# Kernel tuning notes

Measured on AMD Instinct MI355X. Metric: run time of the kernel, lower is better.

## Reference

```python
import jax, jax.numpy as jnp
import numpy as np

N = 50000
E = 800000
HEADS = 4
C = 64  # per-head channels
IN = 256
NEG_SLOPE = 0.2


def setup_inputs() -> dict:
    key = jax.random.key(0)
    k = jax.random.split(key, 6)
    x = jax.random.normal(k[0], (N, IN), dtype=jnp.float32)
    edge_index = jax.random.randint(k[1], (2, E), 0, N, dtype=jnp.int64)
    # Glorot-ish scale for weights
    W = jax.random.normal(k[2], (IN, HEADS * C), dtype=jnp.float32) * (1.0 / np.sqrt(IN))
    att_src = jax.random.normal(k[3], (HEADS, C), dtype=jnp.float32) * (1.0 / np.sqrt(C))
    att_dst = jax.random.normal(k[4], (HEADS, C), dtype=jnp.float32) * (1.0 / np.sqrt(C))
    bias = jax.random.normal(k[5], (HEADS * C,), dtype=jnp.float32) * 0.02
    return {"x": x, "edge_index": edge_index, "W": W, "att_src": att_src,
            "att_dst": att_dst, "bias": bias}


def _gat_forward(x, edge_index, W, att_src, att_dst, bias):
    n = x.shape[0]
    h = (x @ W).reshape(n, HEADS, C)  # [N, H, C]

    # add self loops (PyG default add_self_loops=True)
    loop = jnp.arange(n, dtype=edge_index.dtype)
    src = jnp.concatenate([edge_index[0], loop])  # [E+N]
    dst = jnp.concatenate([edge_index[1], loop])

    # per-node attention contributions  [N, H]
    a_src = jnp.einsum('nhc,hc->nh', h, att_src)
    a_dst = jnp.einsum('nhc,hc->nh', h, att_dst)

    # edge logits with leaky relu  [E+N, H]
    logits = a_src[src] + a_dst[dst]
    logits = jnp.where(logits >= 0, logits, NEG_SLOPE * logits)

    # segment softmax over destination neighborhoods
    seg_max = jax.ops.segment_max(logits, dst, num_segments=n)  # [N, H]
    seg_max = jnp.where(jnp.isfinite(seg_max), seg_max, 0.0)
    ex = jnp.exp(logits - seg_max[dst])
    denom = jax.ops.segment_sum(ex, dst, num_segments=n)  # [N, H]
    alpha = ex / (denom[dst] + 1e-16)  # [E+N, H]

    # weighted scatter-add of source messages
    msgs = alpha[:, :, None] * h[src]  # [E+N, H, C]
    out = jax.ops.segment_sum(msgs, dst, num_segments=n)  # [N, H, C]
    out = out.reshape(n, HEADS * C) + bias
    return jax.nn.relu(out)


def reference(x, edge_index, W, att_src, att_dst, bias):
    return _gat_forward(x, edge_index, W, att_src, att_dst, bias)
```

## Files before the change

kernel.cpp:

```cpp
#include <hip/hip_runtime.h>
#include <hip/hip_bf16.h>
#include <math.h>

#define NEG 0.2f
#define BSH 6
#define EPB 4096

typedef __attribute__((ext_vector_type(4))) float f4;
typedef __attribute__((ext_vector_type(8))) short s8;

__device__ __forceinline__ short f2bf(float f) {
    unsigned u = __float_as_uint(f);
    u += 0x7fff + ((u >> 16) & 1);
    return (short)(u >> 16);
}
__device__ __forceinline__ unsigned pk2(float a, float b) {
    union { __hip_bfloat162 h; unsigned u; } c;
    c.h = __float22bfloat162_rn(make_float2(a, b));
    return c.u;
}
__device__ __forceinline__ float bf2f(unsigned short s) {
    return __uint_as_float(((unsigned)s) << 16);
}

__global__ __launch_bounds__(256) void prep_count(
    const float* __restrict__ W, short* __restrict__ Wt, int* __restrict__ off,
    const int* __restrict__ ei, int* __restrict__ hist2d,
    int E, int N, int NBUCK, int NB, int Etot)
{
    const int blk = blockIdx.x, t = threadIdx.x;
    if (blk < 256) {
        int id = blk * 256 + t;
        int n = id >> 8, k = id & 255;
        Wt[id] = f2bf(W[k * 256 + n]);
        if (id == 0) off[N] = Etot;
        return;
    }
    extern __shared__ int lh[];
    const int cblk = blk - 256;
    for (int b = t; b < NBUCK; b += 256) lh[b] = 0;
    __syncthreads();
    const int e0 = cblk * EPB;
    if (e0 + EPB <= E) {
#pragma unroll
        for (int i = 0; i < EPB / 1024; ++i) {
            int e = e0 + i * 1024 + t * 4;
            int4 d = *(const int4*)(ei + E + e);
            atomicAdd(&lh[d.x >> BSH], 1);
            atomicAdd(&lh[d.y >> BSH], 1);
            atomicAdd(&lh[d.z >> BSH], 1);
            atomicAdd(&lh[d.w >> BSH], 1);
        }
    } else {
        for (int i = 0; i < EPB / 256; ++i) {
            int e = e0 + i * 256 + t;
            if (e < Etot) {
                int dte = (e < E) ? ei[E + e] : (e - E);
                atomicAdd(&lh[dte >> BSH], 1);
            }
        }
    }
    __syncthreads();
    for (int b = t; b < NBUCK; b += 256) hist2d[b * NB + cblk] = lh[b];
}

__global__ __launch_bounds__(1024) void scan1(const int* __restrict__ src,
                                              int* __restrict__ dstT,
                                              int* __restrict__ bsum,
                                              int Ntot, int NB, int NBUCK)
{
    __shared__ int wsum[16], wexc[16];
    const int t = threadIdx.x, lane = t & 63, w = t >> 6;
    const int idx = blockIdx.x * 1024 + t;
    int v = (idx < Ntot) ? src[idx] : 0;
    int val = v;
#pragma unroll
    for (int o = 1; o < 64; o <<= 1) {
        int u = __shfl_up(val, o);
        if (lane >= o) val += u;
    }
    if (lane == 63) wsum[w] = val;
    __syncthreads();
    if (t < 16) {
        int s = wsum[t];
#pragma unroll
        for (int o = 1; o < 16; o <<= 1) {
            int u = __shfl_up(s, o, 16);
            if (t >= o) s += u;
        }
        wexc[t] = s - wsum[t];
        if (t == 15) bsum[blockIdx.x] = s;
    }
    __syncthreads();
    if (idx < Ntot) {
        int b = idx / NB, cblk = idx - b * NB;
        dstT[(size_t)cblk * NBUCK + b] = wexc[w] + val - v;
    }
}

__device__ __forceinline__ void bexc_scan_wave(const int* __restrict__ bsum,
                                               int* bexc_l, int NCH, int t)
{
    if (t < 64) {
        int carry = 0;
        for (int base = 0; base < NCH; base += 64) {
            int i = base + t;
            int v = (i < NCH) ? bsum[i] : 0;
            int val = v;
#pragma unroll
            for (int o = 1; o < 64; o <<= 1) {
                int u = __shfl_up(val, o);
                if (t >= o) val += u;
            }
            if (i < NCH) bexc_l[i] = carry + val - v;
            carry += __shfl(val, 63);
        }
    }
}

__global__ __launch_bounds__(512) void gemm_scatter(
    const float* __restrict__ x, const short* __restrict__ Wt,
    const float* __restrict__ att_src, const float* __restrict__ att_dst,
    short* __restrict__ hb, float* __restrict__ a_src_n,
    float* __restrict__ a_dst_n, int M,
    const int* __restrict__ ei, const int* __restrict__ scannedT,
    const int* __restrict__ bsum, unsigned* __restrict__ bucketed,
    int E, int N, int NBUCK, int NB, int NCH)
{
    extern __shared__ __align__(16) char smem[];
    const int t = threadIdx.x;

    if (blockIdx.x < NB) {
        int* bexc_l = (int*)smem;
        int* lcur   = (int*)smem + 256;
        const int cblk = blockIdx.x;
        bexc_scan_wave(bsum, bexc_l, NCH, t);
        __syncthreads();
        const int* srow = scannedT + (size_t)cblk * NBUCK;
        for (int b = t; b < NBUCK; b += 512)
            lcur[b] = srow[b] + bexc_l[(b * NB + cblk) >> 10];
        __syncthreads();
        const int e0 = cblk * EPB, Etot = E + N;
        if (e0 + EPB <= E) {
#pragma unroll
            for (int i = 0; i < EPB / 2048; ++i) {
                int e = e0 + i * 2048 + t * 4;
                int4 s4 = *(const int4*)(ei + e);
                int4 d4 = *(const int4*)(ei + E + e);
                int p0 = atomicAdd(&lcur[d4.x >> BSH], 1);
                bucketed[p0] = (unsigned)s4.x | ((unsigned)(d4.x & 63) << 20);
                int p1 = atomicAdd(&lcur[d4.y >> BSH], 1);
                bucketed[p1] = (unsigned)s4.y | ((unsigned)(d4.y & 63) << 20);
                int p2 = atomicAdd(&lcur[d4.z >> BSH], 1);
                bucketed[p2] = (unsigned)s4.z | ((unsigned)(d4.z & 63) << 20);
                int p3 = atomicAdd(&lcur[d4.w >> BSH], 1);
                bucketed[p3] = (unsigned)s4.w | ((unsigned)(d4.w & 63) << 20);
            }
        } else {
            for (int i = 0; i < EPB / 512; ++i) {
                int e = e0 + i * 512 + t;
                if (e < Etot) {
                    int src, dte;
                    if (e < E) { src = ei[e]; dte = ei[E + e]; }
                    else       { src = e - E; dte = src; }
                    int pos = atomicAdd(&lcur[dte >> BSH], 1);
                    bucketed[pos] = (unsigned)src | ((unsigned)(dte & 63) << 20);
                }
            }
        }
        return;
    }

    short (*xs)[128][32] = (short (*)[128][32])smem;
    const int lane = t & 63, wv = t >> 6;
    const int wr = wv >> 2;
    const int hd = wv & 3;
    const int quad = lane >> 4, l15 = lane & 15;
    const int n0 = (blockIdx.x - NB) * 128;

    const int row = t >> 2, kq = t & 3;
    const bool okr = (n0 + row) < M;
    const float* xp = x + (size_t)(n0 + row) * 256 + kq * 8;

    const short* wbase = Wt + (size_t)(hd * 64 + l15) * 256 + quad * 8;

    f4 acc[4][4];
#pragma unroll
    for (int i = 0; i < 4; ++i)
#pragma unroll
        for (int j = 0; j < 4; ++j) acc[i][j] = (f4)(0.f);

    float4 v0 = {}, v1 = {};
    if (okr) { const float4* p = (const float4*)xp; v0 = p[0]; v1 = p[1]; }

    s8 af[4];
#pragma unroll
    for (int i = 0; i < 4; ++i)
        af[i] = *(const s8*)(wbase + (size_t)(i * 16) * 256);

    int buf = 0;
#pragma unroll
    for (int ks = 0; ks < 8; ++ks) {
        uint4 u = { pk2(v0.x, v0.y), pk2(v0.z, v0.w), pk2(v1.x, v1.y), pk2(v1.z, v1.w) };
        *(uint4*)&xs[buf][row][kq * 8] = u;
        __syncthreads();

        if (ks < 7 && okr) {
            const float4* p = (const float4*)(xp + (ks + 1) * 32);
            v0 = p[0]; v1 = p[1];
        }

        s8 afn[4];
        if (ks < 7) {
#pragma unroll
            for (int i = 0; i < 4; ++i)
                afn[i] = *(const s8*)(wbase + (size_t)(i * 16) * 256 + (ks + 1) * 32);
        }

        s8 bf[4];
#pragma unroll
        for (int j = 0; j < 4; ++j)
            bf[j] = *(const s8*)&xs[buf][wr * 64 + j * 16 + l15][quad * 8];
#pragma unroll
        for (int i = 0; i < 4; ++i)
#pragma unroll
            for (int j = 0; j < 4; ++j)
                acc[i][j] = __builtin_amdgcn_mfma_f32_16x16x32_bf16(af[i], bf[j], acc[i][j], 0, 0, 0);

        if (ks < 7) {
#pragma unroll
            for (int i = 0; i < 4; ++i) af[i] = afn[i];
        }
        buf ^= 1;
    }

    float asv[4][4], adv[4][4];
#pragma unroll
    for (int i = 0; i < 4; ++i)
#pragma unroll
        for (int rr = 0; rr < 4; ++rr) {
            asv[i][rr] = att_src[hd * 64 + i * 16 + quad * 4 + rr];
            adv[i][rr] = att_dst[hd * 64 + i * 16 + quad * 4 + rr];
        }

#pragma unroll
    for (int j = 0; j < 4; ++j) {
        const int node = n0 + wr * 64 + j * 16 + l15;
        const bool ok = node < M;
        float ps = 0.f, pd = 0.f;
#pragma unroll
        for (int i = 0; i < 4; ++i)
#pragma unroll
            for (int rr = 0; rr < 4; ++rr) {
                float v = acc[i][j][rr];
                ps = fmaf(v, asv[i][rr], ps);
                pd = fmaf(v, adv[i][rr], pd);
            }
        ps += __shfl_xor(ps, 16); ps += __shfl_xor(ps, 32);
        pd += __shfl_xor(pd, 16); pd += __shfl_xor(pd, 32);
        if (ok && quad == 0) {
            a_src_n[node * 4 + hd] = ps;
            a_dst_n[node * 4 + hd] = pd;
        }
        if (ok) {
#pragma unroll
            for (int i = 0; i < 4; ++i) {
                uint2 pk = make_uint2(pk2(acc[i][j][0], acc[i][j][1]),
                                      pk2(acc[i][j][2], acc[i][j][3]));
                *(uint2*)&hb[(size_t)node * 256 + hd * 64 + i * 16 + quad * 4] = pk;
            }
        }
    }
}

__global__ __launch_bounds__(256) void csr_build(
    const unsigned* __restrict__ bucketed, const int* __restrict__ scannedT,
    const int* __restrict__ bsum, int* __restrict__ off, int* __restrict__ csr,
    int N, int NB, int NBUCK, int Etot, int NCH)
{
    __shared__ unsigned est[2048];
    __shared__ int ldeg4[4][64], lcur4[4][64], loff[64], bexc_l[192];
    const int t = threadIdx.x, wv = t >> 6, b = blockIdx.x;

    bexc_scan_wave(bsum, bexc_l, NCH, t);
    ldeg4[t >> 6][t & 63] = 0;
    __syncthreads();

    const int gbase = scannedT[b] + bexc_l[(b * NB) >> 10];
    int gend;
    if (b + 1 == NBUCK) gend = Etot;
    else gend = scannedT[b + 1] + bexc_l[((b + 1) * NB) >> 10];
    int cnt = gend - gbase;
    if (cnt > 2048) cnt = 2048;

    for (int i = t; i < cnt; i += 256) {
        unsigned en = bucketed[gbase + i];
        est[i] = en;
        atomicAdd(&ldeg4[wv][en >> 20], 1);
    }
    __syncthreads();
    if (t < 64) {
        int d0 = ldeg4[0][t], d1 = ldeg4[1][t], d2 = ldeg4[2][t], d3 = ldeg4[3][t];
        int tot = d0 + d1 + d2 + d3;
        int val = tot;
#pragma unroll
        for (int o = 1; o < 64; o <<= 1) {
            int u = __shfl_up(val, o);
            if (t >= o) val += u;
        }
        int excl = val - tot;
        loff[t] = excl;
        lcur4[0][t] = excl;
        lcur4[1][t] = excl + d0;
        lcur4[2][t] = excl + d0 + d1;
        lcur4[3][t] = excl + d0 + d1 + d2;
    }
    __syncthreads();
    for (int i = t; i < cnt; i += 256) {
        unsigned en = est[i];
        int pos = atomicAdd(&lcur4[wv][en >> 20], 1);
        csr[gbase + pos] = (int)(en & 0xFFFFF);
    }
    if (t < 64) {
        int n = (b << BSH) + t;
        if (n < N) off[n] = gbase + loff[t];
    }
}

__global__ __launch_bounds__(256) void aggregate(const short* __restrict__ hb,
                                                 const float* __restrict__ a_src_n,
                                                 const float* __restrict__ a_dst_n,
                                                 const int* __restrict__ off,
                                                 const int* __restrict__ csr,
                                                 const float* __restrict__ bias,
                                                 float* __restrict__ out, int N)
{
    __shared__ float lds_w[4][64][4];
    __shared__ int   lds_s[4][64];
    const int wv = threadIdx.x >> 6;
    const int lane = threadIdx.x & 63;
    const int half = lane >> 5, l31 = lane & 31;
    const int n = blockIdx.x * 4 + wv;
    if (n >= N) return;

    const int base = off[n];
    const int d = off[n + 1] - base;
    const float4 ad = *(const float4*)(a_dst_n + 4 * n);
    const int hl = l31 >> 3;

    float acc[8] = {0.f, 0.f, 0.f, 0.f, 0.f, 0.f, 0.f, 0.f};
    float4 sum = make_float4(0.f, 0.f, 0.f, 0.f);
    const uint4* hp = (const uint4*)hb;

    for (int c0 = 0; c0 < d; c0 += 64) {
        int j = c0 + lane;
        int s = 0;
        float4 w4 = make_float4(0.f, 0.f, 0.f, 0.f);
        if (j < d) {
            s = csr[base + j];
            float4 as = *(const float4*)(a_src_n + 4 * s);
            float lx = as.x + ad.x; lx = lx >= 0.f ? lx : NEG * lx;
            float ly = as.y + ad.y; ly = ly >= 0.f ? ly : NEG * ly;
            float lz = as.z + ad.z; lz = lz >= 0.f ? lz : NEG * lz;
            float lw = as.w + ad.w; lw = lw >= 0.f ? lw : NEG * lw;
            w4 = make_float4(__expf(lx), __expf(ly), __expf(lz), __expf(lw));
        }
        sum.x += w4.x; sum.y += w4.y; sum.z += w4.z; sum.w += w4.w;
        *(float4*)&lds_w[wv][lane][0] = w4;
        lds_s[wv][lane] = s;
        __builtin_amdgcn_wave_barrier();

        const int cl = (d - c0) < 64 ? (d - c0) : 64;
        int jj = 0;
        for (; jj + 4 <= cl; jj += 4) {
            int   s0 = lds_s[wv][jj + half];
            int   s1 = lds_s[wv][jj + 2 + half];
            float w0 = lds_w[wv][jj + half][hl];
            float w1 = lds_w[wv][jj + 2 + half][hl];
            uint4 v0 = hp[(size_t)s0 * 32 + l31];
            uint4 v1 = hp[(size_t)s1 * 32 + l31];
            acc[0] = fmaf(w0, bf2f((unsigned short)(v0.x & 0xffff)), acc[0]);
            acc[1] = fmaf(w0, bf2f((unsigned short)(v0.x >> 16)),    acc[1]);
            acc[2] = fmaf(w0, bf2f((unsigned short)(v0.y & 0xffff)), acc[2]);
            acc[3] = fmaf(w0, bf2f((unsigned short)(v0.y >> 16)),    acc[3]);
            acc[4] = fmaf(w0, bf2f((unsigned short)(v0.z & 0xffff)), acc[4]);
            acc[5] = fmaf(w0, bf2f((unsigned short)(v0.z >> 16)),    acc[5]);
            acc[6] = fmaf(w0, bf2f((unsigned short)(v0.w & 0xffff)), acc[6]);
            acc[7] = fmaf(w0, bf2f((unsigned short)(v0.w >> 16)),    acc[7]);
            acc[0] = fmaf(w1, bf2f((unsigned short)(v1.x & 0xffff)), acc[0]);
            acc[1] = fmaf(w1, bf2f((unsigned short)(v1.x >> 16)),    acc[1]);
            acc[2] = fmaf(w1, bf2f((unsigned short)(v1.y & 0xffff)), acc[2]);
            acc[3] = fmaf(w1, bf2f((unsigned short)(v1.y >> 16)),    acc[3]);
            acc[4] = fmaf(w1, bf2f((unsigned short)(v1.z & 0xffff)), acc[4]);
            acc[5] = fmaf(w1, bf2f((unsigned short)(v1.z >> 16)),    acc[5]);
            acc[6] = fmaf(w1, bf2f((unsigned short)(v1.w & 0xffff)), acc[6]);
            acc[7] = fmaf(w1, bf2f((unsigned short)(v1.w >> 16)),    acc[7]);
        }
        for (; jj < cl; jj += 2) {
            int   s0 = lds_s[wv][jj + half];
            float w0 = lds_w[wv][jj + half][hl];
            uint4 v0 = hp[(size_t)s0 * 32 + l31];
            acc[0] = fmaf(w0, bf2f((unsigned short)(v0.x & 0xffff)), acc[0]);
            acc[1] = fmaf(w0, bf2f((unsigned short)(v0.x >> 16)),    acc[1]);
            acc[2] = fmaf(w0, bf2f((unsigned short)(v0.y & 0xffff)), acc[2]);
            acc[3] = fmaf(w0, bf2f((unsigned short)(v0.y >> 16)),    acc[3]);
            acc[4] = fmaf(w0, bf2f((unsigned short)(v0.z & 0xffff)), acc[4]);
            acc[5] = fmaf(w0, bf2f((unsigned short)(v0.z >> 16)),    acc[5]);
            acc[6] = fmaf(w0, bf2f((unsigned short)(v0.w & 0xffff)), acc[6]);
            acc[7] = fmaf(w0, bf2f((unsigned short)(v0.w >> 16)),    acc[7]);
        }
        __builtin_amdgcn_wave_barrier();
    }

#pragma unroll
    for (int k = 0; k < 8; ++k) acc[k] += __shfl_xor(acc[k], 32);

#pragma unroll
    for (int o = 32; o > 0; o >>= 1) {
        sum.x += __shfl_xor(sum.x, o);
        sum.y += __shfl_xor(sum.y, o);
        sum.z += __shfl_xor(sum.z, o);
        sum.w += __shfl_xor(sum.w, o);
    }
    float sh = (hl & 2) ? ((hl & 1) ? sum.w : sum.z) : ((hl & 1) ? sum.y : sum.x);
    float ih = 1.f / (sh + 1e-16f);

    if (half == 0) {
        const float4* bp = (const float4*)bias + l31 * 2;
        float4 b0 = bp[0], b1 = bp[1];
        float4 o0, o1;
        o0.x = fmaxf(fmaf(acc[0], ih, b0.x), 0.f);
        o0.y = fmaxf(fmaf(acc[1], ih, b0.y), 0.f);
        o0.z = fmaxf(fmaf(acc[2], ih, b0.z), 0.f);
        o0.w = fmaxf(fmaf(acc[3], ih, b0.w), 0.f);
        o1.x = fmaxf(fmaf(acc[4], ih, b1.x), 0.f);
        o1.y = fmaxf(fmaf(acc[5], ih, b1.y), 0.f);
        o1.z = fmaxf(fmaf(acc[6], ih, b1.z), 0.f);
        o1.w = fmaxf(fmaf(acc[7], ih, b1.w), 0.f);
        float4* op = (float4*)(out + (size_t)n * 256) + l31 * 2;
        op[0] = o0;
        op[1] = o1;
    }
}

extern "C" void kernel_launch(void* const* d_in, const int* in_sizes, int n_in,
                              void* d_out, int out_size, void* d_ws, size_t ws_size,
                              hipStream_t stream)
{
    const float* x       = (const float*)d_in[0];
    const int*   ei      = (const int*)d_in[1];
    const float* W       = (const float*)d_in[2];
    const float* att_src = (const float*)d_in[3];
    const float* att_dst = (const float*)d_in[4];
    const float* bias    = (const float*)d_in[5];
    float* out = (float*)d_out;

    const int N = in_sizes[0] / 256;
    const int E = in_sizes[1] / 2;
    const int Etot = E + N;
    const int NBUCK = (N + 63) >> BSH;
    const int NB = (Etot + EPB - 1) / EPB;
    const int Ntot = NBUCK * NB;
    const int NCH = (Ntot + 1023) / 1024;
    const int GB = (N + 127) / 128;

    char* p = (char*)d_ws;
    short*    hb      = (short*)p;    p += (size_t)N * 256 * sizeof(short);
    short*    Wt      = (short*)p;    p += 256 * 256 * sizeof(short);
    float*    a_src_n = (float*)p;    p += (size_t)N * 4 * sizeof(float);
    float*    a_dst_n = (float*)p;    p += (size_t)N * 4 * sizeof(float);
    int*      hist2d  = (int*)p;      p += (size_t)Ntot * sizeof(int);
    int*      scannedT= (int*)p;      p += (size_t)Ntot * sizeof(int);
    int*      bsum    = (int*)p;      p += 1024 * sizeof(int);
    int*      off     = (int*)p;      p += (size_t)(N + 1) * sizeof(int);
    unsigned* bucketed= (unsigned*)p; p += (size_t)Etot * sizeof(unsigned);
    int*      csr     = (int*)p;      p += (size_t)Etot * sizeof(int);

    prep_count<<<256 + NB, 256, NBUCK * sizeof(int), stream>>>(
        W, Wt, off, ei, hist2d, E, N, NBUCK, NB, Etot);
    scan1<<<NCH, 1024, 0, stream>>>(hist2d, scannedT, bsum, Ntot, NB, NBUCK);
    gemm_scatter<<<NB + GB, 512, 16384, stream>>>(
        x, Wt, att_src, att_dst, hb, a_src_n, a_dst_n, N,
        ei, scannedT, bsum, bucketed, E, N, NBUCK, NB, NCH);
    csr_build<<<NBUCK, 256, 0, stream>>>(bucketed, scannedT, bsum, off, csr,
                                         N, NB, NBUCK, Etot, NCH);
    aggregate<<<(N + 3) / 4, 256, 0, stream>>>(hb, a_src_n, a_dst_n, off, csr,
                                               bias, out, N);
}
```

Measured before the change: 218.7 us.

## Halve edges per scatter block, place GEMM blocks first, widen csr_build to 512 threads

```diff
diff --git a/kernel.cpp b/kernel.cpp
--- a/kernel.cpp
+++ b/kernel.cpp
@@ -4,7 +4,7 @@
 
 #define NEG 0.2f
 #define BSH 6
-#define EPB 4096
+#define EPB 2048
 
 typedef __attribute__((ext_vector_type(4))) float f4;
 typedef __attribute__((ext_vector_type(8))) short s8;
@@ -122,7 +122,7 @@
     const float* __restrict__ x, const short* __restrict__ Wt,
     const float* __restrict__ att_src, const float* __restrict__ att_dst,
     short* __restrict__ hb, float* __restrict__ a_src_n,
-    float* __restrict__ a_dst_n, int M,
+    float* __restrict__ a_dst_n, int M, int GB,
     const int* __restrict__ ei, const int* __restrict__ scannedT,
     const int* __restrict__ bsum, unsigned* __restrict__ bucketed,
     int E, int N, int NBUCK, int NB, int NCH)
@@ -130,10 +130,10 @@
     extern __shared__ __align__(16) char smem[];
     const int t = threadIdx.x;
 
-    if (blockIdx.x < NB) {
+    if (blockIdx.x >= GB) {
         int* bexc_l = (int*)smem;
-        int* lcur   = (int*)smem + 256;
-        const int cblk = blockIdx.x;
+        int* lcur   = (int*)smem + 384;
+        const int cblk = blockIdx.x - GB;
         bexc_scan_wave(bsum, bexc_l, NCH, t);
         __syncthreads();
         const int* srow = scannedT + (size_t)cblk * NBUCK;
@@ -142,20 +142,17 @@
         __syncthreads();
         const int e0 = cblk * EPB, Etot = E + N;
         if (e0 + EPB <= E) {
-#pragma unroll
-            for (int i = 0; i < EPB / 2048; ++i) {
-                int e = e0 + i * 2048 + t * 4;
-                int4 s4 = *(const int4*)(ei + e);
-                int4 d4 = *(const int4*)(ei + E + e);
-                int p0 = atomicAdd(&lcur[d4.x >> BSH], 1);
-                bucketed[p0] = (unsigned)s4.x | ((unsigned)(d4.x & 63) << 20);
-                int p1 = atomicAdd(&lcur[d4.y >> BSH], 1);
-                bucketed[p1] = (unsigned)s4.y | ((unsigned)(d4.y & 63) << 20);
-                int p2 = atomicAdd(&lcur[d4.z >> BSH], 1);
-                bucketed[p2] = (unsigned)s4.z | ((unsigned)(d4.z & 63) << 20);
-                int p3 = atomicAdd(&lcur[d4.w >> BSH], 1);
-                bucketed[p3] = (unsigned)s4.w | ((unsigned)(d4.w & 63) << 20);
-            }
+            int e = e0 + t * 4;
+            int4 s4 = *(const int4*)(ei + e);
+            int4 d4 = *(const int4*)(ei + E + e);
+            int p0 = atomicAdd(&lcur[d4.x >> BSH], 1);
+            bucketed[p0] = (unsigned)s4.x | ((unsigned)(d4.x & 63) << 20);
+            int p1 = atomicAdd(&lcur[d4.y >> BSH], 1);
+            bucketed[p1] = (unsigned)s4.y | ((unsigned)(d4.y & 63) << 20);
+            int p2 = atomicAdd(&lcur[d4.z >> BSH], 1);
+            bucketed[p2] = (unsigned)s4.z | ((unsigned)(d4.z & 63) << 20);
+            int p3 = atomicAdd(&lcur[d4.w >> BSH], 1);
+            bucketed[p3] = (unsigned)s4.w | ((unsigned)(d4.w & 63) << 20);
         } else {
             for (int i = 0; i < EPB / 512; ++i) {
                 int e = e0 + i * 512 + t;
@@ -176,7 +173,7 @@
     const int wr = wv >> 2;
     const int hd = wv & 3;
     const int quad = lane >> 4, l15 = lane & 15;
-    const int n0 = (blockIdx.x - NB) * 128;
+    const int n0 = blockIdx.x * 128;
 
     const int row = t >> 2, kq = t & 3;
     const bool okr = (n0 + row) < M;
@@ -273,17 +270,17 @@
     }
 }
 
-__global__ __launch_bounds__(256) void csr_build(
+__global__ __launch_bounds__(512) void csr_build(
     const unsigned* __restrict__ bucketed, const int* __restrict__ scannedT,
     const int* __restrict__ bsum, int* __restrict__ off, int* __restrict__ csr,
     int N, int NB, int NBUCK, int Etot, int NCH)
 {
     __shared__ unsigned est[2048];
-    __shared__ int ldeg4[4][64], lcur4[4][64], loff[64], bexc_l[192];
+    __shared__ int ldeg8[8][64], lcur8[8][64], loff[64], bexc_l[384];
     const int t = threadIdx.x, wv = t >> 6, b = blockIdx.x;
 
     bexc_scan_wave(bsum, bexc_l, NCH, t);
-    ldeg4[t >> 6][t & 63] = 0;
+    ldeg8[t >> 6][t & 63] = 0;
     __syncthreads();
 
     const int gbase = scannedT[b] + bexc_l[(b * NB) >> 10];
@@ -293,15 +290,16 @@
     int cnt = gend - gbase;
     if (cnt > 2048) cnt = 2048;
 
-    for (int i = t; i < cnt; i += 256) {
+    for (int i = t; i < cnt; i += 512) {
         unsigned en = bucketed[gbase + i];
         est[i] = en;
-        atomicAdd(&ldeg4[wv][en >> 20], 1);
+        atomicAdd(&ldeg8[wv][en >> 20], 1);
     }
     __syncthreads();
     if (t < 64) {
-        int d0 = ldeg4[0][t], d1 = ldeg4[1][t], d2 = ldeg4[2][t], d3 = ldeg4[3][t];
-        int tot = d0 + d1 + d2 + d3;
+        int d0 = ldeg8[0][t], d1 = ldeg8[1][t], d2 = ldeg8[2][t], d3 = ldeg8[3][t];
+        int d4 = ldeg8[4][t], d5 = ldeg8[5][t], d6 = ldeg8[6][t], d7 = ldeg8[7][t];
+        int tot = d0 + d1 + d2 + d3 + d4 + d5 + d6 + d7;
         int val = tot;
 #pragma unroll
         for (int o = 1; o < 64; o <<= 1) {
@@ -310,15 +308,20 @@
         }
         int excl = val - tot;
         loff[t] = excl;
-        lcur4[0][t] = excl;
-        lcur4[1][t] = excl + d0;
-        lcur4[2][t] = excl + d0 + d1;
-        lcur4[3][t] = excl + d0 + d1 + d2;
-    }
-    __syncthreads();
-    for (int i = t; i < cnt; i += 256) {
+        int c = excl;
+        lcur8[0][t] = c; c += d0;
+        lcur8[1][t] = c; c += d1;
+        lcur8[2][t] = c; c += d2;
+        lcur8[3][t] = c; c += d3;
+        lcur8[4][t] = c; c += d4;
+        lcur8[5][t] = c; c += d5;
+        lcur8[6][t] = c; c += d6;
+        lcur8[7][t] = c;
+    }
+    __syncthreads();
+    for (int i = t; i < cnt; i += 512) {
         unsigned en = est[i];
-        int pos = atomicAdd(&lcur4[wv][en >> 20], 1);
+        int pos = atomicAdd(&lcur8[wv][en >> 20], 1);
         csr[gbase + pos] = (int)(en & 0xFFFFF);
     }
     if (t < 64) {
@@ -479,10 +482,10 @@
     prep_count<<<256 + NB, 256, NBUCK * sizeof(int), stream>>>(
         W, Wt, off, ei, hist2d, E, N, NBUCK, NB, Etot);
     scan1<<<NCH, 1024, 0, stream>>>(hist2d, scannedT, bsum, Ntot, NB, NBUCK);
-    gemm_scatter<<<NB + GB, 512, 16384, stream>>>(
-        x, Wt, att_src, att_dst, hb, a_src_n, a_dst_n, N,
+    gemm_scatter<<<GB + NB, 512, 16384, stream>>>(
+        x, Wt, att_src, att_dst, hb, a_src_n, a_dst_n, N, GB,
         ei, scannedT, bsum, bucketed, E, N, NBUCK, NB, NCH);
-    csr_build<<<NBUCK, 256, 0, stream>>>(bucketed, scannedT, bsum, off, csr,
+    csr_build<<<NBUCK, 512, 0, stream>>>(bucketed, scannedT, bsum, off, csr,
                                          N, NB, NBUCK, Etot, NCH);
     aggregate<<<(N + 3) / 4, 256, 0, stream>>>(hb, a_src_n, a_dst_n, off, csr,
                                                bias, out, N);
```

After: 217.4 us. Within noise of the previous version (-0.6%).
